# Kernel tuning notes

Measured on AMD Instinct MI355X. Metric: run time of the kernel, lower is better.

## Reference

```python
import jax, jax.numpy as jnp
import numpy as np
import math

NH, NKV, D = 32, 8, 128  # query heads, kv heads, head_dim
ROPE_THETA = 10000.0


def _rotate_half(x):
    x1, x2 = jnp.split(x, 2, axis=-1)
    return jnp.concatenate([-x2, x1], axis=-1)


def _rope_cache(position_ids):
    # position_ids: [B, S] int -> cos, sin: [B, S, D]
    inv_freq = 1.0 / (ROPE_THETA ** (jnp.arange(0, D, 2, dtype=jnp.float32) / D))
    freqs = position_ids.astype(jnp.float32)[..., None] * inv_freq  # [B,S,D/2]
    emb = jnp.concatenate([freqs, freqs], axis=-1)  # [B,S,D]
    return jnp.cos(emb), jnp.sin(emb)


def setup_inputs() -> dict:
    key = jax.random.key(0)
    k0, k1, k2, k3, k4 = jax.random.split(key, 5)
    B, S, H = 1, 2048, 4096
    scale = 0.02
    return {
        "hidden_states": jax.random.normal(k0, (B, S, H), jnp.float32),
        "position_ids": jnp.broadcast_to(jnp.arange(S, dtype=jnp.int32), (B, S)),
        "Wq": jax.random.normal(k1, (H, NH * D), jnp.float32) * scale,
        "Wk": jax.random.normal(k2, (H, NKV * D), jnp.float32) * scale,
        "Wv": jax.random.normal(k3, (H, NKV * D), jnp.float32) * scale,
        "Wo": jax.random.normal(k4, (NH * D, H), jnp.float32) * scale,
    }


def reference(hidden_states, position_ids, Wq, Wk, Wv, Wo):
    B, S, H = hidden_states.shape
    # QKV projections, move heads front: [B, H, S, D]
    Q = (hidden_states @ Wq).reshape(B, S, NH, D).transpose(0, 2, 1, 3)
    K = (hidden_states @ Wk).reshape(B, S, NKV, D).transpose(0, 2, 1, 3)
    V = (hidden_states @ Wv).reshape(B, S, NKV, D).transpose(0, 2, 1, 3)
    # RoPE
    cos, sin = _rope_cache(position_ids)  # [B,S,D]
    cos, sin = cos[:, None], sin[:, None]  # broadcast over heads
    Q = Q * cos + _rotate_half(Q) * sin
    K = K * cos + _rotate_half(K) * sin
    # GQA: repeat kv heads to match query heads
    g = NH // NKV
    K = jnp.repeat(K, g, axis=1)
    V = jnp.repeat(V, g, axis=1)
    # scaled QK^T with causal mask (mask=True -> keep, else finfo.min)
    scores = jnp.einsum("bhqd,bhkd->bhqk", Q, K) / math.sqrt(D)
    causal = jnp.tril(jnp.ones((S, S), dtype=bool))
    scores = jnp.where(causal, scores, jnp.finfo(scores.dtype).min)
    probs = jax.nn.softmax(scores.astype(jnp.float32), axis=-1).astype(Q.dtype)
    attn = jnp.einsum("bhqk,bhkd->bhqd", probs, V)
    attn = attn.transpose(0, 2, 1, 3).reshape(B, S, NH * D)
    return attn @ Wo
```

## Files before the change

kernel.cpp:

```cpp
#include <hip/hip_runtime.h>
#include <hip/hip_bf16.h>
#include <math.h>

typedef __bf16 bf16;
typedef __bf16 bf16x4 __attribute__((ext_vector_type(4)));
typedef __bf16 bf16x8 __attribute__((ext_vector_type(8)));
typedef float f32x4 __attribute__((ext_vector_type(4)));

#define GLB __attribute__((address_space(1)))
#define LDSAS __attribute__((address_space(3)))

__global__ void probe_dtype(const unsigned int* __restrict__ X, int* __restrict__ flag) {
  int t = threadIdx.x;
  int cnt = 0;
  for (int i = t; i < 512; i += 64) {
    unsigned int e = (X[i] >> 7) & 0xFF;
    cnt += (e >= 110 && e <= 135) ? 1 : 0;
  }
#pragma unroll
  for (int off = 32; off > 0; off >>= 1) cnt += __shfl_down(cnt, off, 64);
  if (t == 0) flag[0] = (cnt < 256) ? 1 : 0;
}

__global__ void prep_weights(const void* __restrict__ Wq, const void* __restrict__ Wk,
                             const void* __restrict__ Wv, const void* __restrict__ Wo,
                             const void* __restrict__ X,
                             bf16* __restrict__ Wqkvt, bf16* __restrict__ Wot,
                             bf16* __restrict__ Xb, const int* __restrict__ flag) {
  const int f = flag[0];
  const int tx = threadIdx.x, ty = threadIdx.y;
  __shared__ bf16 tile[32][34];
  int b = blockIdx.x;
  const void* W;
  bf16* out;
  int N, bx, by;
  if (b < 16384) {
    W = Wq; out = Wqkvt; N = 4096; bx = b & 127; by = b >> 7;
  } else if (b < 20480) {
    b -= 16384; W = Wk; out = Wqkvt + (size_t)4096 * 4096; N = 1024; bx = b & 31; by = b >> 5;
  } else if (b < 24576) {
    b -= 20480; W = Wv; out = Wqkvt + (size_t)5120 * 4096; N = 1024; bx = b & 31; by = b >> 5;
  } else if (b < 40960) {
    b -= 24576; W = Wo; out = Wot; N = 4096; bx = b & 127; by = b >> 7;
  } else {
    b -= 40960;
    const int t = ty * 8 + tx;
    const size_t i = ((size_t)b * 256 + t) * 4;
    bf16x4 o;
    if (f) {
      const float4 v = *(const float4*)((const float*)X + i);
      o[0] = (bf16)v.x; o[1] = (bf16)v.y; o[2] = (bf16)v.z; o[3] = (bf16)v.w;
    } else {
      o = *(const bf16x4*)((const bf16*)X + i);
    }
    *(bf16x4*)&Xb[i] = o;
    return;
  }
  const int n0 = bx * 32, k0 = by * 32;
  if (f) {
    const float4 v = *(const float4*)((const float*)W + (size_t)(k0 + ty) * N + n0 + 4 * tx);
    tile[ty][4 * tx + 0] = (bf16)v.x;
    tile[ty][4 * tx + 1] = (bf16)v.y;
    tile[ty][4 * tx + 2] = (bf16)v.z;
    tile[ty][4 * tx + 3] = (bf16)v.w;
  } else {
    const bf16x4 v = *(const bf16x4*)((const bf16*)W + (size_t)(k0 + ty) * N + n0 + 4 * tx);
#pragma unroll
    for (int u = 0; u < 4; ++u) tile[ty][4 * tx + u] = v[u];
  }
  __syncthreads();
  bf16x4 o;
#pragma unroll
  for (int u = 0; u < 4; ++u) o[u] = tile[4 * tx + u][ty];
  *(bf16x4*)&out[(size_t)(n0 + ty) * 4096 + k0 + 4 * tx] = o;
}

__global__ __launch_bounds__(256, 2) void gemm_bt(
    const bf16* __restrict__ A, const bf16* __restrict__ Bt,
    void* __restrict__ C, const int* __restrict__ flagp, int M, int N, int K) {
  __shared__ bf16 As[128 * 32];
  __shared__ bf16 Bs[128 * 32];
  const int t = threadIdx.x;
  const int m0 = blockIdx.y * 128, n0 = blockIdx.x * 128;
  const int lane = t & 63, n16 = lane & 15, quad = lane >> 4;
  const int w = t >> 6, wrow = w >> 1, wcol = w & 1;

  f32x4 acc[4][4] = {};
  const int colA = (((t & 3) ^ ((t >> 3) & 3))) * 8;
  const int rA = t >> 2;
  const int sw = (n16 >> 1) & 3;
  const int rdoff = ((quad ^ sw) * 8);

  for (int k0 = 0; k0 < K; k0 += 32) {
#pragma unroll
    for (int i = 0; i < 2; ++i) {
      const int elem = i * 2048 + t * 8;
      const int row = i * 64 + rA;
      __builtin_amdgcn_global_load_lds(
          (const GLB void*)(A + (size_t)(m0 + row) * K + k0 + colA),
          (LDSAS void*)(&As[elem]), 16, 0, 0);
      __builtin_amdgcn_global_load_lds(
          (const GLB void*)(Bt + (size_t)(n0 + row) * K + k0 + colA),
          (LDSAS void*)(&Bs[elem]), 16, 0, 0);
    }
    __syncthreads();
    bf16x8 af[4], bfr[4];
#pragma unroll
    for (int i = 0; i < 4; ++i) {
      af[i] = *(const bf16x8*)&As[(wrow * 64 + i * 16 + n16) * 32 + rdoff];
      bfr[i] = *(const bf16x8*)&Bs[(wcol * 64 + i * 16 + n16) * 32 + rdoff];
    }
#pragma unroll
    for (int mi = 0; mi < 4; ++mi)
#pragma unroll
      for (int ni = 0; ni < 4; ++ni)
        acc[mi][ni] = __builtin_amdgcn_mfma_f32_16x16x32_bf16(
            af[mi], bfr[ni], acc[mi][ni], 0, 0, 0);
    __syncthreads();
  }
  const bool f32out = (flagp != nullptr) && (flagp[0] != 0);
  if (f32out) {
    float* Cf = (float*)C;
#pragma unroll
    for (int mi = 0; mi < 4; ++mi)
#pragma unroll
      for (int ni = 0; ni < 4; ++ni) {
        const int r0 = m0 + wrow * 64 + mi * 16 + quad * 4;
        const int c = n0 + wcol * 64 + ni * 16 + n16;
#pragma unroll
        for (int r = 0; r < 4; ++r) Cf[(size_t)(r0 + r) * N + c] = acc[mi][ni][r];
      }
  } else {
    bf16* Cb = (bf16*)C;
#pragma unroll
    for (int mi = 0; mi < 4; ++mi)
#pragma unroll
      for (int ni = 0; ni < 4; ++ni) {
        const int r0 = m0 + wrow * 64 + mi * 16 + quad * 4;
        const int c = n0 + wcol * 64 + ni * 16 + n16;
#pragma unroll
        for (int r = 0; r < 4; ++r) Cb[(size_t)(r0 + r) * N + c] = (bf16)acc[mi][ni][r];
      }
  }
}

__global__ void rope_vt(bf16* __restrict__ QKV, const int* __restrict__ pos,
                        bf16* __restrict__ Vt) {
  const int t = threadIdx.x;
  int b = blockIdx.x;
  if (b < 20480) {
    const int idx = b * 256 + t;
    const int i = idx & 63;
    const int hh = (idx >> 6) % 40;
    const int s = idx / (64 * 40);
    bf16* px = QKV + (size_t)s * 6144 + hh * 128 + i;
    const float x1 = (float)px[0], x2 = (float)px[64];
    const float p = (float)pos[s];
    const float inv = exp2f((float)i * -0.2076205088f);
    float sn, cs;
    sincosf(p * inv, &sn, &cs);
    px[0] = (bf16)(x1 * cs - x2 * sn);
    px[64] = (bf16)(x2 * cs + x1 * sn);
  } else {
    b -= 20480;
    __shared__ bf16 tile[32][34];
    const int tx = t & 31, ty = t >> 5;
    const int v0 = (b & 31) * 32, s0 = (b >> 5) * 32;
#pragma unroll
    for (int j = 0; j < 4; ++j)
      tile[ty + j * 8][tx] = QKV[(size_t)(s0 + ty + j * 8) * 6144 + 5120 + v0 + tx];
    __syncthreads();
#pragma unroll
    for (int j = 0; j < 4; ++j)
      Vt[(size_t)(v0 + ty + j * 8) * 2048 + s0 + tx] = tile[tx][ty + j * 8];
  }
}

__global__ __launch_bounds__(256) void flash_attn(
    const bf16* __restrict__ QKV, const bf16* __restrict__ Vt_g,
    bf16* __restrict__ O) {
  __shared__ bf16 Ks[2][64 * 128];
  __shared__ bf16 Vs[2][128 * 64];
  __shared__ bf16 Ps[64 * 72];
  const int pairp = blockIdx.x;
  const int h = blockIdx.y, hkv = h >> 2;
  const int t = threadIdx.x, w = t >> 6, lane = t & 63;
  const int n16 = lane & 15, quad = lane >> 4;
  const bf16* Qp = QKV + h * 128;
  const bf16* Kp = QKV + 4096 + hkv * 128;
  const bf16* Vp = Vt_g + (size_t)hkv * 128 * 2048;

  const int krow = t >> 4, kg = t & 15;
  const int vd = t >> 3, vg = t & 7;

  for (int pass = 0; pass < 2; ++pass) {
    const int qt = (pass == 0) ? pairp : 31 - pairp;
    bf16x8 qa[4];
    {
      const bf16* qrow = Qp + (size_t)(qt * 64 + w * 16 + n16) * 6144 + quad * 8;
#pragma unroll
      for (int kf = 0; kf < 4; ++kf) qa[kf] = *(const bf16x8*)(qrow + kf * 32);
    }
    f32x4 o[8] = {};
    float l_[4] = {0.f, 0.f, 0.f, 0.f};

    __syncthreads();

    auto stage = [&](int kt, int buf) {
#pragma unroll
      for (int j = 0; j < 4; ++j) {
        const int row = j * 16 + krow;
        const int g = kg ^ (row & 7);
        __builtin_amdgcn_global_load_lds(
            (const GLB void*)(Kp + (size_t)(kt * 64 + row) * 6144 + g * 8),
            (LDSAS void*)(&Ks[buf][j * 2048 + t * 8]), 16, 0, 0);
      }
#pragma unroll
      for (int j = 0; j < 4; ++j) {
        const int d = j * 32 + vd;
        const int g = vg ^ (d & 7);
        __builtin_amdgcn_global_load_lds(
            (const GLB void*)(Vp + (size_t)d * 2048 + kt * 64 + g * 8),
            (LDSAS void*)(&Vs[buf][j * 2048 + t * 8]), 16, 0, 0);
      }
    };

    stage(0, 0);
    for (int kt = 0; kt <= qt; ++kt) {
      const int cur = kt & 1;
      __syncthreads();
      if (kt < qt) stage(kt + 1, cur ^ 1);

      float p[4][4];
      const bool diag = (kt == qt);
      const int s7 = n16 & 7;
#pragma unroll
      for (int ns = 0; ns < 4; ++ns) {
        f32x4 c = {};
#pragma unroll
        for (int kf = 0; kf < 4; ++kf)
          c = __builtin_amdgcn_mfma_f32_16x16x32_bf16(
              qa[kf],
              *(const bf16x8*)&Ks[cur][(ns * 16 + n16) * 128 +
                                       (((kf * 4 + quad) ^ s7) * 8)],
              c, 0, 0, 0);
        if (diag) {
          const int kvi = ns * 16 + n16;
          const int ql = w * 16 + quad * 4;
#pragma unroll
          for (int r = 0; r < 4; ++r)
            p[ns][r] = (kvi > ql + r)
                           ? 0.f
                           : __expf(fminf(c[r] * 0.08838834764831845f, 60.f));
        } else {
#pragma unroll
          for (int r = 0; r < 4; ++r)
            p[ns][r] = __expf(fminf(c[r] * 0.08838834764831845f, 60.f));
        }
      }
#pragma unroll
      for (int r = 0; r < 4; ++r)
        l_[r] += (p[0][r] + p[1][r]) + (p[2][r] + p[3][r]);
#pragma unroll
      for (int ns = 0; ns < 4; ++ns)
#pragma unroll
        for (int r = 0; r < 4; ++r)
          Ps[(w * 16 + quad * 4 + r) * 72 + ns * 16 + n16] = (bf16)p[ns][r];
      const bf16x8 a0 = *(const bf16x8*)&Ps[(w * 16 + n16) * 72 + quad * 8];
      const bf16x8 a1 = *(const bf16x8*)&Ps[(w * 16 + n16) * 72 + 32 + quad * 8];
#pragma unroll
      for (int dt = 0; dt < 8; ++dt) {
        const int d = dt * 16 + n16;
        const bf16x8 b0 = *(const bf16x8*)&Vs[cur][d * 64 + ((quad ^ s7) * 8)];
        o[dt] = __builtin_amdgcn_mfma_f32_16x16x32_bf16(a0, b0, o[dt], 0, 0, 0);
        const bf16x8 b1 = *(const bf16x8*)&Vs[cur][d * 64 + (((4 + quad) ^ s7) * 8)];
        o[dt] = __builtin_amdgcn_mfma_f32_16x16x32_bf16(a1, b1, o[dt], 0, 0, 0);
      }
    }
#pragma unroll
    for (int r = 0; r < 4; ++r) {
#pragma unroll
      for (int off = 1; off < 16; off <<= 1) l_[r] += __shfl_xor(l_[r], off, 64);
    }
    float linv[4];
#pragma unroll
    for (int r = 0; r < 4; ++r) linv[r] = 1.f / l_[r];
#pragma unroll
    for (int dt = 0; dt < 8; ++dt)
#pragma unroll
      for (int r = 0; r < 4; ++r) {
        const int qi = qt * 64 + w * 16 + quad * 4 + r;
        O[(size_t)qi * 4096 + h * 128 + dt * 16 + n16] = (bf16)(o[dt][r] * linv[r]);
      }
  }
}

extern "C" void kernel_launch(void* const* d_in, const int* in_sizes, int n_in,
                              void* d_out, int out_size, void* d_ws, size_t ws_size,
                              hipStream_t stream) {
  (void)in_sizes; (void)n_in; (void)out_size; (void)ws_size;
  const void* X = d_in[0];
  const int* pos = (const int*)d_in[1];
  const void* Wq = d_in[2];
  const void* Wk = d_in[3];
  const void* Wv = d_in[4];
  const void* Wo = d_in[5];

  char* ws = (char*)d_ws;
  const size_t MB = 1ull << 20;
  int* flag   = (int*)(ws + 0);
  bf16* Xb    = (bf16*)(ws + 1 * MB);
  bf16* attn  = (bf16*)(ws + 1 * MB);
  bf16* Wqkvt = (bf16*)(ws + 17 * MB);
  bf16* Wot   = (bf16*)(ws + 65 * MB);
  bf16* QKV   = (bf16*)(ws + 97 * MB);
  bf16* Vt_g  = (bf16*)(ws + 121 * MB);

  probe_dtype<<<1, 64, 0, stream>>>((const unsigned int*)X, flag);

  prep_weights<<<49152, dim3(8, 32), 0, stream>>>(Wq, Wk, Wv, Wo, X,
                                                  Wqkvt, Wot, Xb, flag);

  gemm_bt<<<dim3(48, 16), 256, 0, stream>>>(Xb, Wqkvt, QKV, nullptr, 2048, 6144, 4096);

  rope_vt<<<22528, 256, 0, stream>>>(QKV, pos, Vt_g);

  flash_attn<<<dim3(16, 32), 256, 0, stream>>>(QKV, Vt_g, attn);

  gemm_bt<<<dim3(32, 16), 256, 0, stream>>>(attn, Wot, d_out, flag, 2048, 4096, 4096);
}
```

Baseline: 495.6 us.

## Replace GEMM with 256-row double-buffered 8-wave MFMA kernel

Replaces the 128x128 single-buffered GEMM with a templated 512-thread kernel using 256xBN tiles and a K step of 64. It double-buffers LDS, prefetching the next K tile with global_load_lds while the current tile feeds MFMAs, and uses an XOR swizzle, explicit vmcnt waits and setprio around the MFMA phases. The goals are more data reuse per block, fewer barriers and overlap of global loads with compute. The trade-off is much higher LDS use per block and fewer blocks: the QKV projection launches only 192 blocks, which may leave some CUs idle.

```diff
diff --git a/kernel.cpp b/kernel.cpp
--- a/kernel.cpp
+++ b/kernel.cpp
@@ -75,71 +75,116 @@
   *(bf16x4*)&out[(size_t)(n0 + ty) * 4096 + k0 + 4 * tx] = o;
 }
 
-__global__ __launch_bounds__(256, 2) void gemm_bt(
+template <int BN>
+__global__ __launch_bounds__(512, 2) void gemm8(
     const bf16* __restrict__ A, const bf16* __restrict__ Bt,
-    void* __restrict__ C, const int* __restrict__ flagp, int M, int N, int K) {
-  __shared__ bf16 As[128 * 32];
-  __shared__ bf16 Bs[128 * 32];
+    void* __restrict__ C, const int* __restrict__ flagp,
+    int M, int N, int K) {
+  constexpr int NF  = BN / 64;
+  constexpr int NB  = BN / 64;
+  constexpr int LPT = 4 + NB;
+  __shared__ __attribute__((aligned(16))) bf16 As[2][256 * 64];
+  __shared__ __attribute__((aligned(16))) bf16 Bs[2][BN * 64];
+
   const int t = threadIdx.x;
-  const int m0 = blockIdx.y * 128, n0 = blockIdx.x * 128;
-  const int lane = t & 63, n16 = lane & 15, quad = lane >> 4;
-  const int w = t >> 6, wrow = w >> 1, wcol = w & 1;
-
-  f32x4 acc[4][4] = {};
-  const int colA = (((t & 3) ^ ((t >> 3) & 3))) * 8;
-  const int rA = t >> 2;
-  const int sw = (n16 >> 1) & 3;
-  const int rdoff = ((quad ^ sw) * 8);
-
-  for (int k0 = 0; k0 < K; k0 += 32) {
-#pragma unroll
-    for (int i = 0; i < 2; ++i) {
-      const int elem = i * 2048 + t * 8;
-      const int row = i * 64 + rA;
-      __builtin_amdgcn_global_load_lds(
-          (const GLB void*)(A + (size_t)(m0 + row) * K + k0 + colA),
-          (LDSAS void*)(&As[elem]), 16, 0, 0);
-      __builtin_amdgcn_global_load_lds(
-          (const GLB void*)(Bt + (size_t)(n0 + row) * K + k0 + colA),
-          (LDSAS void*)(&Bs[elem]), 16, 0, 0);
-    }
-    __syncthreads();
-    bf16x8 af[4], bfr[4];
-#pragma unroll
-    for (int i = 0; i < 4; ++i) {
-      af[i] = *(const bf16x8*)&As[(wrow * 64 + i * 16 + n16) * 32 + rdoff];
-      bfr[i] = *(const bf16x8*)&Bs[(wcol * 64 + i * 16 + n16) * 32 + rdoff];
-    }
-#pragma unroll
-    for (int mi = 0; mi < 4; ++mi)
-#pragma unroll
-      for (int ni = 0; ni < 4; ++ni)
-        acc[mi][ni] = __builtin_amdgcn_mfma_f32_16x16x32_bf16(
-            af[mi], bfr[ni], acc[mi][ni], 0, 0, 0);
-    __syncthreads();
-  }
+  const int w = t >> 6, lane = t & 63;
+  const int n16 = lane & 15, quad = lane >> 4;
+  const int wr = w >> 2, wc = w & 3;
+  const int m0 = blockIdx.y * 256, n0 = blockIdx.x * BN;
+  (void)M;
+
+  f32x4 acc[8][NF] = {};
+
+  const int srow = t >> 3;
+  const int scol = ((t & 7) ^ (srow & 7)) * 8;
+  const bf16* pa[4];
+  const bf16* pb[NB];
+#pragma unroll
+  for (int i = 0; i < 4; ++i) pa[i] = A + (size_t)(m0 + i * 64 + srow) * K + scol;
+#pragma unroll
+  for (int i = 0; i < NB; ++i) pb[i] = Bt + (size_t)(n0 + i * 64 + srow) * K + scol;
+
+  auto stage = [&](int kt, int buf) {
+    const int koff = kt * 64;
+#pragma unroll
+    for (int i = 0; i < 4; ++i)
+      __builtin_amdgcn_global_load_lds((const GLB void*)(pa[i] + koff),
+                                       (LDSAS void*)(&As[buf][i * 4096 + t * 8]),
+                                       16, 0, 0);
+#pragma unroll
+    for (int i = 0; i < NB; ++i)
+      __builtin_amdgcn_global_load_lds((const GLB void*)(pb[i] + koff),
+                                       (LDSAS void*)(&Bs[buf][i * 4096 + t * 8]),
+                                       16, 0, 0);
+  };
+
+  const int nt = K >> 6;
+  const int rdk = n16 & 7;
+
+  stage(0, 0);
+  for (int kt = 0; kt < nt; ++kt) {
+    const int cur = kt & 1;
+    if (kt + 1 < nt) {
+      stage(kt + 1, cur ^ 1);
+      if constexpr (LPT == 8)
+        asm volatile("s_waitcnt vmcnt(8)" ::: "memory");
+      else
+        asm volatile("s_waitcnt vmcnt(6)" ::: "memory");
+    } else {
+      asm volatile("s_waitcnt vmcnt(0)" ::: "memory");
+    }
+    __builtin_amdgcn_s_barrier();
+    const bf16* Asb = &As[cur][0];
+    const bf16* Bsb = &Bs[cur][0];
+#pragma unroll
+    for (int ph = 0; ph < 4; ++ph) {
+      const int mh = ph >> 1, ks = ph & 1;
+      bf16x8 af[4], bfv[NF];
+#pragma unroll
+      for (int mf = 0; mf < 4; ++mf)
+        af[mf] = *(const bf16x8*)&Asb[(wr * 128 + mh * 64 + mf * 16 + n16) * 64 +
+                                      (((ks * 4 + quad) ^ rdk) * 8)];
+#pragma unroll
+      for (int nf = 0; nf < NF; ++nf)
+        bfv[nf] = *(const bf16x8*)&Bsb[(wc * (BN / 4) + nf * 16 + n16) * 64 +
+                                       (((ks * 4 + quad) ^ rdk) * 8)];
+      __builtin_amdgcn_s_barrier();
+      asm volatile("s_waitcnt lgkmcnt(0)" ::: "memory");
+      __builtin_amdgcn_sched_barrier(0);
+      __builtin_amdgcn_s_setprio(1);
+#pragma unroll
+      for (int mf = 0; mf < 4; ++mf)
+#pragma unroll
+        for (int nf = 0; nf < NF; ++nf)
+          acc[mh * 4 + mf][nf] = __builtin_amdgcn_mfma_f32_16x16x32_bf16(
+              af[mf], bfv[nf], acc[mh * 4 + mf][nf], 0, 0, 0);
+      __builtin_amdgcn_s_setprio(0);
+      __builtin_amdgcn_s_barrier();
+    }
+  }
+
   const bool f32out = (flagp != nullptr) && (flagp[0] != 0);
   if (f32out) {
     float* Cf = (float*)C;
 #pragma unroll
-    for (int mi = 0; mi < 4; ++mi)
-#pragma unroll
-      for (int ni = 0; ni < 4; ++ni) {
-        const int r0 = m0 + wrow * 64 + mi * 16 + quad * 4;
-        const int c = n0 + wcol * 64 + ni * 16 + n16;
-#pragma unroll
-        for (int r = 0; r < 4; ++r) Cf[(size_t)(r0 + r) * N + c] = acc[mi][ni][r];
+    for (int mi = 0; mi < 8; ++mi)
+#pragma unroll
+      for (int nf = 0; nf < NF; ++nf) {
+        const int r0 = m0 + wr * 128 + (mi >> 2) * 64 + (mi & 3) * 16 + quad * 4;
+        const int c = n0 + wc * (BN / 4) + nf * 16 + n16;
+#pragma unroll
+        for (int r = 0; r < 4; ++r) Cf[(size_t)(r0 + r) * N + c] = acc[mi][nf][r];
       }
   } else {
     bf16* Cb = (bf16*)C;
 #pragma unroll
-    for (int mi = 0; mi < 4; ++mi)
-#pragma unroll
-      for (int ni = 0; ni < 4; ++ni) {
-        const int r0 = m0 + wrow * 64 + mi * 16 + quad * 4;
-        const int c = n0 + wcol * 64 + ni * 16 + n16;
-#pragma unroll
-        for (int r = 0; r < 4; ++r) Cb[(size_t)(r0 + r) * N + c] = (bf16)acc[mi][ni][r];
+    for (int mi = 0; mi < 8; ++mi)
+#pragma unroll
+      for (int nf = 0; nf < NF; ++nf) {
+        const int r0 = m0 + wr * 128 + (mi >> 2) * 64 + (mi & 3) * 16 + quad * 4;
+        const int c = n0 + wc * (BN / 4) + nf * 16 + n16;
+#pragma unroll
+        for (int r = 0; r < 4; ++r) Cb[(size_t)(r0 + r) * N + c] = (bf16)acc[mi][nf][r];
       }
   }
 }
@@ -321,11 +366,11 @@
   prep_weights<<<49152, dim3(8, 32), 0, stream>>>(Wq, Wk, Wv, Wo, X,
                                                   Wqkvt, Wot, Xb, flag);
 
-  gemm_bt<<<dim3(48, 16), 256, 0, stream>>>(Xb, Wqkvt, QKV, nullptr, 2048, 6144, 4096);
+  gemm8<256><<<dim3(24, 8), 512, 0, stream>>>(Xb, Wqkvt, QKV, nullptr, 2048, 6144, 4096);
 
   rope_vt<<<22528, 256, 0, stream>>>(QKV, pos, Vt_g);
 
   flash_attn<<<dim3(16, 32), 256, 0, stream>>>(QKV, Vt_g, attn);
 
-  gemm_bt<<<dim3(32, 16), 256, 0, stream>>>(attn, Wot, d_out, flag, 2048, 4096, 4096);
-}
+  gemm8<128><<<dim3(32, 8), 512, 0, stream>>>(attn, Wot, d_out, flag, 2048, 4096, 4096);
+}
```

New measurement: 550.5 us. 11.1% more time.
